# Kernel optimization log

Hardware: AMD Instinct MI355X
Metric: run time of the kernel (lower is better)

The kernel has to match this reference:

```python
import jax, jax.numpy as jnp
import numpy as np

N = 3072      # packed vision tokens (multiple of _BLOCK=128, so no padding needed)
D = 1280      # hidden_size
H = 16        # num_heads
K = 80        # head_dim = D // H
NSEG = 8      # number of packed images/segments


def setup_inputs() -> dict:
    key = jax.random.key(0)
    ks = jax.random.split(key, 8)
    hidden_ND = jax.random.normal(ks[0], (N, D), jnp.float32)
    inner = jnp.sort(jax.random.randint(ks[1], (NSEG - 1,), 1, N)).astype(jnp.int32)
    cu_seqlens = jnp.concatenate([
        jnp.zeros((1,), jnp.int32), inner, jnp.full((1,), N, jnp.int32)])
    theta = jax.random.uniform(ks[2], (N, K), jnp.float32, 0.0, 2.0 * np.pi)
    cos_NK = jnp.cos(theta)
    sin_NK = jnp.sin(theta)
    sd = 1.0 / np.sqrt(D)  # lecun_normal-ish scale
    qkv_w = jax.random.normal(ks[3], (D, 3 * D), jnp.float32) * sd
    qkv_b = jax.random.normal(ks[4], (3 * D,), jnp.float32) * 0.01
    proj_w = jax.random.normal(ks[5], (D, D), jnp.float32) * sd
    proj_b = jax.random.normal(ks[6], (D,), jnp.float32) * 0.01
    return {"hidden_ND": hidden_ND, "cu_seqlens": cu_seqlens,
            "cos_NK": cos_NK, "sin_NK": sin_NK,
            "qkv_w": qkv_w, "qkv_b": qkv_b,
            "proj_w": proj_w, "proj_b": proj_b}


def _rotate_half(x):
    x1, x2 = jnp.split(x, 2, axis=-1)
    return jnp.concatenate([-x2, x1], axis=-1)


def _apply_vision_rope(q_NHK, k_NHK, cos_NK, sin_NK):
    c = cos_NK[:, None, :]  # (N, 1, K) broadcast over heads
    s = sin_NK[:, None, :]
    q = q_NHK * c + _rotate_half(q_NHK) * s
    k = k_NHK * c + _rotate_half(k_NHK) * s
    return q, k


def reference(hidden_ND, cu_seqlens, cos_NK, sin_NK, qkv_w, qkv_b, proj_w, proj_b):
    n = hidden_ND.shape[0]
    scale = K ** (-0.5)
    qkv = (hidden_ND @ qkv_w + qkv_b).reshape(n, 3, H, K)
    q_NHK, k_NHK, v_NHK = qkv[:, 0], qkv[:, 1], qkv[:, 2]
    q_NHK, k_NHK = _apply_vision_rope(q_NHK, k_NHK, cos_NK, sin_NK)

    # segment-boundary mask: token i attends to [k_start[i], k_end[i])
    idx = jnp.arange(n)
    seg = jnp.searchsorted(cu_seqlens[1:], idx, side='right')
    nseg = cu_seqlens.shape[0]
    k_start = cu_seqlens[jnp.minimum(seg, nseg - 2)]
    k_end = cu_seqlens[jnp.minimum(seg + 1, nseg - 1)]
    mask = (idx[None, :] >= k_start[:, None]) & (idx[None, :] < k_end[:, None])  # (Nq, Nk)

    scores = jnp.einsum('nhk,mhk->hnm', q_NHK, k_NHK) * scale  # (H, N, N)
    scores = jnp.where(mask[None], scores, jnp.float32(-1e30))
    probs = jax.nn.softmax(scores, axis=-1)
    attn = jnp.einsum('hnm,mhk->nhk', probs, v_NHK)  # (N, H, K)
    out_ND = attn.reshape(n, H * K) @ proj_w + proj_b
    return out_ND
```

## Files before the change

kernel.cpp:

```cpp
#include <hip/hip_runtime.h>

#define NTOK 3072
#define DM   1280
#define NH   16
#define HD   80
#define HDS  104
#define KVB  128
#define NSEG 8
#define QKVC 3840

typedef __attribute__((ext_vector_type(4))) float  f32x4;
typedef __attribute__((ext_vector_type(8))) __bf16 bf16x8;
typedef __attribute__((ext_vector_type(8))) unsigned short ushort8;
typedef __attribute__((ext_vector_type(4))) unsigned short ushort4v;

static __device__ __forceinline__ unsigned short f2bf(float f){
  union{float f; unsigned int u;} v; v.f=f;
  unsigned int r = v.u + 0x7fffu + ((v.u>>16)&1u);
  return (unsigned short)(r>>16);
}
static __device__ __forceinline__ float bf2f(unsigned short u){
  union{unsigned int i; float f;} v; v.i = ((unsigned int)u)<<16; return v.f;
}
static __device__ __forceinline__ void gload_lds16(const void* g, void* l){
  __builtin_amdgcn_global_load_lds((const __attribute__((address_space(1))) void*)g,
                                   (__attribute__((address_space(3))) void*)l, 16, 0, 0);
}

__global__ void cast_f32_bf16(const float* __restrict__ src, unsigned short* __restrict__ dst, int n){
  int i = (blockIdx.x*256 + threadIdx.x)*4;
  if (i >= n) return;
  f32x4 v = *reinterpret_cast<const f32x4*>(&src[i]);
  ushort4v o;
  o[0]=f2bf(v[0]); o[1]=f2bf(v[1]); o[2]=f2bf(v[2]); o[3]=f2bf(v[3]);
  *reinterpret_cast<ushort4v*>(&dst[i]) = o;
}

__global__ void transpose_cast(const float* __restrict__ src, unsigned short* __restrict__ dst, int R, int C){
  __shared__ unsigned short tile[32][33];
  int c0 = blockIdx.x*32, r0 = blockIdx.y*32;
  int tx = threadIdx.x, ty = threadIdx.y;
  #pragma unroll
  for (int i=0;i<4;i++){
    int r = r0 + ty + i*8;
    tile[ty+i*8][tx] = f2bf(src[(size_t)r*C + c0 + tx]);
  }
  __syncthreads();
  #pragma unroll
  for (int i=0;i<4;i++){
    int c = c0 + ty + i*8;
    dst[(size_t)c*R + r0 + tx] = tile[tx][ty+i*8];
  }
}

__global__ void transpose_v(const unsigned short* __restrict__ qkv, unsigned short* __restrict__ Vt){
  __shared__ unsigned short tile[32][33];
  int n0 = blockIdx.x*32, d0 = blockIdx.y*32, h = blockIdx.z;
  int tx = threadIdx.x, ty = threadIdx.y;
  #pragma unroll
  for (int i=0;i<4;i++){
    int n = n0 + ty + i*8;
    int d = d0 + tx;
    tile[ty+i*8][tx] = (d < HD) ? qkv[(size_t)n*QKVC + 2*DM + h*HD + d] : (unsigned short)0;
  }
  __syncthreads();
  #pragma unroll
  for (int i=0;i<4;i++){
    int d = d0 + ty + i*8;
    if (d < HD) Vt[((size_t)h*HD + d)*NTOK + n0 + tx] = tile[tx][ty+i*8];
  }
}

template<int OUT_BF16>
__global__ __launch_bounds__(256) void gemm_bt(
    const unsigned short* __restrict__ A,
    const unsigned short* __restrict__ Bt,
    const float* __restrict__ bias,
    unsigned short* __restrict__ Cb,
    float* __restrict__ Cf,
    int M, int Ncol, int Kd)
{
  __shared__ unsigned short As[128*32];
  __shared__ unsigned short Bs[128*32];
  const int tid  = threadIdx.x;
  const int lane = tid & 63, wave = tid >> 6;
  const int wr = wave >> 1, wc = wave & 1;
  const int bm = blockIdx.y, bn = blockIdx.x;
  const f32x4 vzero = {0.f,0.f,0.f,0.f};

  f32x4 acc[4][4];
  #pragma unroll
  for (int i=0;i<4;i++)
    #pragma unroll
    for (int j=0;j<4;j++) acc[i][j] = vzero;

  const int rsub = lane>>2;
  const int kc   = (lane&3)*8;
  const unsigned short* Ab = A  + (size_t)(bm*128 + wave*32 + rsub)*Kd + kc;
  const unsigned short* Bb = Bt + (size_t)(bn*128 + wave*32 + rsub)*Kd + kc;

  for (int k0=0; k0<Kd; k0+=32){
    __syncthreads();
    #pragma unroll
    for (int i=0;i<2;i++){
      gload_lds16(Ab + (size_t)i*16*Kd + k0, &As[(wave*2+i)*512]);
      gload_lds16(Bb + (size_t)i*16*Kd + k0, &Bs[(wave*2+i)*512]);
    }
    __syncthreads();
    bf16x8 a[4], b[4];
    #pragma unroll
    for (int mf=0; mf<4; mf++)
      a[mf] = *reinterpret_cast<const bf16x8*>(&As[(wr*64 + mf*16 + (lane&15))*32 + ((lane>>4)<<3)]);
    #pragma unroll
    for (int nf=0; nf<4; nf++)
      b[nf] = *reinterpret_cast<const bf16x8*>(&Bs[(wc*64 + nf*16 + (lane&15))*32 + ((lane>>4)<<3)]);
    #pragma unroll
    for (int mf=0; mf<4; mf++)
      #pragma unroll
      for (int nf=0; nf<4; nf++)
        acc[mf][nf] = __builtin_amdgcn_mfma_f32_16x16x32_bf16(a[mf], b[nf], acc[mf][nf], 0,0,0);
  }

  const int crow0 = bm*128 + wr*64;
  const int ccol0 = bn*128 + wc*64;
  #pragma unroll
  for (int nf=0; nf<4; nf++){
    int col = ccol0 + nf*16 + (lane&15);
    float bv = bias[col];
    #pragma unroll
    for (int mf=0; mf<4; mf++){
      #pragma unroll
      for (int r=0;r<4;r++){
        int row = crow0 + mf*16 + ((lane>>4)<<2) + r;
        float v = acc[mf][nf][r] + bv;
        if (OUT_BF16) Cb[(size_t)row*Ncol + col] = f2bf(v);
        else          Cf[(size_t)row*Ncol + col] = v;
      }
    }
  }
}

__global__ void rope_repack(const unsigned short* __restrict__ qkv,
                            const float* __restrict__ cosNK, const float* __restrict__ sinNK,
                            unsigned short* __restrict__ Qr, unsigned short* __restrict__ Kr)
{
  int idx = blockIdx.x*256 + threadIdx.x;
  if (idx >= NH*NTOK*HDS) return;
  int k  = idx % HDS;
  int nh = idx / HDS;
  int n  = nh % NTOK;
  int h  = nh / NTOK;
  size_t dsti = (size_t)(h*NTOK + n)*HDS + k;
  if (k >= HD){ Qr[dsti]=0; Kr[dsti]=0; return; }
  float c = cosNK[n*HD + k], s = sinNK[n*HD + k];
  int   kp  = (k < 40) ? (k+40) : (k-40);
  float sgn = (k < 40) ? -1.f : 1.f;
  size_t base = (size_t)n*QKVC + h*HD;
  float q   = bf2f(qkv[base + k]);
  float qp  = bf2f(qkv[base + kp]);
  float kk  = bf2f(qkv[base + DM + k]);
  float kkp = bf2f(qkv[base + DM + kp]);
  Qr[dsti] = f2bf(q*c  + sgn*qp*s);
  Kr[dsti] = f2bf(kk*c + sgn*kkp*s);
}

__global__ __launch_bounds__(256) void attn_kernel(
    const unsigned short* __restrict__ Qr,
    const unsigned short* __restrict__ Kr,
    const unsigned short* __restrict__ Vt,
    const int* __restrict__ cu,
    unsigned short* __restrict__ attn_out)
{
  __shared__ unsigned short Qs[64*HDS];
  __shared__ unsigned short Ks[KVB*HDS];
  __shared__ unsigned short Vs[HD*KVB];
  __shared__ unsigned short Ps[64*KVB];
  __shared__ int rs[64], re[64];

  const int h   = blockIdx.y;
  const int q0  = blockIdx.x*64;
  const int tid = threadIdx.x;
  const int lane = tid & 63, wave = tid >> 6;
  const int l16 = lane & 15, g16 = lane >> 4;
  const f32x4 vzero = {0.f,0.f,0.f,0.f};

  if (tid < 64){
    int row = q0 + tid, seg = 0;
    #pragma unroll
    for (int j=1;j<NSEG;j++) seg += (cu[j] <= row) ? 1 : 0;
    rs[tid] = cu[seg]; re[tid] = cu[seg+1];
  }
  {
    const char* src = (const char*)(Qr + (size_t)(h*NTOK + q0)*HDS);
    #pragma unroll
    for (int i=0;i<4;i++){
      int t = tid + i*256;
      if (t < 832) gload_lds16(src + (size_t)t*16, (char*)Qs + (size_t)t*16);
    }
  }
  __syncthreads();
  const int kmin = rs[0], kmax = re[63];

  f32x4 accO[5];
  #pragma unroll
  for (int i=0;i<5;i++) accO[i] = vzero;
  float m_r[4] = {-1e30f,-1e30f,-1e30f,-1e30f};
  float l_r[4] = {0.f,0.f,0.f,0.f};
  const float scale = 0.11180339887498948f;

  for (int kt = (kmin/KVB)*KVB; kt < kmax; kt += KVB){
    __syncthreads();
    {
      const char* src = (const char*)(Kr + (size_t)(h*NTOK + kt)*HDS);
      #pragma unroll
      for (int i=0;i<7;i++){
        int t = tid + i*256;
        if (t < 1664) gload_lds16(src + (size_t)t*16, (char*)Ks + (size_t)t*16);
      }
    }
    {
      #pragma unroll
      for (int i=0;i<5;i++){
        int t = tid + i*256;
        int row = t >> 4;
        int ch  = (t & 15) ^ (row & 7);
        const unsigned short* src = Vt + ((size_t)h*HD + row)*NTOK + kt + ch*8;
        gload_lds16(src, (char*)Vs + (size_t)t*16);
      }
    }
    __syncthreads();

    f32x4 accS[8];
    #pragma unroll
    for (int i=0;i<8;i++) accS[i] = vzero;
    #pragma unroll
    for (int ks=0; ks<3; ks++){
      bf16x8 aq = *reinterpret_cast<const bf16x8*>((const char*)Qs + (wave*16 + l16)*208 + ks*64 + g16*16);
      #pragma unroll
      for (int nf=0;nf<8;nf++){
        bf16x8 bk = *reinterpret_cast<const bf16x8*>((const char*)Ks + (nf*16 + l16)*208 + ks*64 + g16*16);
        accS[nf] = __builtin_amdgcn_mfma_f32_16x16x32_bf16(aq, bk, accS[nf], 0,0,0);
      }
    }
    #pragma unroll
    for (int r=0;r<4;r++){
      const int row_i = wave*16 + g16*4 + r;
      const int rst = rs[row_i], ren = re[row_i];
      float sv[8]; bool ok[8];
      float mx = -1e30f;
      #pragma unroll
      for (int nf=0;nf<8;nf++){
        int kcol = kt + nf*16 + l16;
        ok[nf] = (kcol >= rst) && (kcol < ren);
        sv[nf] = accS[nf][r]*scale;
        if (ok[nf]) mx = fmaxf(mx, sv[nf]);
      }
      #pragma unroll
      for (int d=1; d<16; d<<=1) mx = fmaxf(mx, __shfl_xor(mx, d, 64));
      float mnew  = fmaxf(m_r[r], mx);
      float alpha = __expf(m_r[r] - mnew);
      m_r[r] = mnew;
      float lsum = 0.f;
      #pragma unroll
      for (int nf=0;nf<8;nf++){
        float p = ok[nf] ? __expf(sv[nf] - mnew) : 0.f;
        int pb = (row_i*256 + nf*32 + l16*2) ^ ((row_i&7)<<4);
        *reinterpret_cast<unsigned short*>((char*)Ps + pb) = f2bf(p);
        lsum += p;
      }
      #pragma unroll
      for (int d=1; d<16; d<<=1) lsum += __shfl_xor(lsum, d, 64);
      l_r[r] = l_r[r]*alpha + lsum;
      #pragma unroll
      for (int cf=0; cf<5; cf++) accO[cf][r] *= alpha;
    }
    #pragma unroll
    for (int ks=0; ks<4; ks++){
      const int arow = wave*16 + l16;
      bf16x8 ap = *reinterpret_cast<const bf16x8*>((char*)Ps + ((arow*256 + ks*64 + g16*16) ^ ((arow&7)<<4)));
      #pragma unroll
      for (int cf=0; cf<5; cf++){
        const int vrow = cf*16 + l16;
        bf16x8 bv = *reinterpret_cast<const bf16x8*>((char*)Vs + ((vrow*256 + ks*64 + g16*16) ^ ((vrow&7)<<4)));
        accO[cf] = __builtin_amdgcn_mfma_f32_16x16x32_bf16(ap, bv, accO[cf], 0,0,0);
      }
    }
  }

  #pragma unroll
  for (int cf=0; cf<5; cf++){
    #pragma unroll
    for (int r=0;r<4;r++){
      int row = q0 + wave*16 + g16*4 + r;
      int col = h*HD + cf*16 + l16;
      attn_out[(size_t)row*DM + col] = f2bf(accO[cf][r] / l_r[r]);
    }
  }
}

extern "C" void kernel_launch(void* const* d_in, const int* in_sizes, int n_in,
                              void* d_out, int out_size, void* d_ws, size_t ws_size,
                              hipStream_t stream)
{
  const float* hidden = (const float*)d_in[0];
  const int*   cu     = (const int*)  d_in[1];
  const float* cosNK  = (const float*)d_in[2];
  const float* sinNK  = (const float*)d_in[3];
  const float* qkv_w  = (const float*)d_in[4];
  const float* qkv_b  = (const float*)d_in[5];
  const float* proj_w = (const float*)d_in[6];
  const float* proj_b = (const float*)d_in[7];
  float* out = (float*)d_out;

  char* w = (char*)d_ws;
  unsigned short* hid_bf  = (unsigned short*)w;  w += (size_t)NTOK*DM*2;
  unsigned short* qkvwT   = (unsigned short*)w;  w += (size_t)QKVC*DM*2;
  unsigned short* projwT  = (unsigned short*)w;  w += (size_t)DM*DM*2;
  unsigned short* qkv_bf  = (unsigned short*)w;  w += (size_t)NTOK*QKVC*2;
  unsigned short* Qr      = (unsigned short*)w;  w += (size_t)NH*NTOK*HDS*2;
  unsigned short* Kr      = (unsigned short*)w;  w += (size_t)NH*NTOK*HDS*2;
  unsigned short* Vt      = qkvwT;
  unsigned short* attn_bf = hid_bf;

  cast_f32_bf16<<<(NTOK*DM/4 + 255)/256, 256, 0, stream>>>(hidden, hid_bf, NTOK*DM);
  transpose_cast<<<dim3(QKVC/32, DM/32), dim3(32,8), 0, stream>>>(qkv_w, qkvwT, DM, QKVC);
  transpose_cast<<<dim3(DM/32,  DM/32), dim3(32,8), 0, stream>>>(proj_w, projwT, DM, DM);
  gemm_bt<1><<<dim3(QKVC/128, NTOK/128), 256, 0, stream>>>(hid_bf, qkvwT, qkv_b, qkv_bf, nullptr, NTOK, QKVC, DM);
  rope_repack<<<(NH*NTOK*HDS + 255)/256, 256, 0, stream>>>(qkv_bf, cosNK, sinNK, Qr, Kr);
  transpose_v<<<dim3(NTOK/32, 3, NH), dim3(32,8), 0, stream>>>(qkv_bf, Vt);
  attn_kernel<<<dim3(NTOK/64, NH), 256, 0, stream>>>(Qr, Kr, Vt, cu, attn_bf);
  gemm_bt<0><<<dim3(DM/128, NTOK/128), 256, 0, stream>>>(attn_bf, projwT, proj_b, nullptr, out, NTOK, DM, DM);
}
```

Measured before the change: 273.2 us.

## Double-buffer GEMM and attention K tiles; load V directly into registers

The GEMM now double-buffers its A/B LDS tiles, issuing the next k-slice's global-to-LDS loads before computing on the current one, so each iteration needs one barrier instead of two. The attention kernel halves the KV block to 64, double-buffers K in LDS with a prefetch of the next tile, and loads V fragments straight from global memory into registers instead of staging them through LDS. It also computes the key range from cu_seqlens directly. The aim is to hide global load latency behind MFMA work and cut barriers, at the cost of more LDS, more registers, more loop iterations, and uncoalesced per-lane V reads from global memory.

After: 268.2 us. No clear change (-1.8%).

```diff
diff --git a/kernel.cpp b/kernel.cpp
--- a/kernel.cpp
+++ b/kernel.cpp
@@ -5,7 +5,7 @@
 #define NH   16
 #define HD   80
 #define HDS  104
-#define KVB  128
+#define KVB  64
 #define NSEG 8
 #define QKVC 3840
 
@@ -80,8 +80,8 @@
     float* __restrict__ Cf,
     int M, int Ncol, int Kd)
 {
-  __shared__ unsigned short As[128*32];
-  __shared__ unsigned short Bs[128*32];
+  __shared__ unsigned short As[2][128*32];
+  __shared__ unsigned short Bs[2][128*32];
   const int tid  = threadIdx.x;
   const int lane = tid & 63, wave = tid >> 6;
   const int wr = wave >> 1, wc = wave & 1;
@@ -99,21 +99,43 @@
   const unsigned short* Ab = A  + (size_t)(bm*128 + wave*32 + rsub)*Kd + kc;
   const unsigned short* Bb = Bt + (size_t)(bn*128 + wave*32 + rsub)*Kd + kc;
 
-  for (int k0=0; k0<Kd; k0+=32){
+  #pragma unroll
+  for (int i=0;i<2;i++){
+    gload_lds16(Ab + (size_t)i*16*Kd, &As[0][(wave*2+i)*512]);
+    gload_lds16(Bb + (size_t)i*16*Kd, &Bs[0][(wave*2+i)*512]);
+  }
+  __syncthreads();
+
+  int cur = 0;
+  for (int k0=32; k0<Kd; k0+=32){
+    #pragma unroll
+    for (int i=0;i<2;i++){
+      gload_lds16(Ab + (size_t)i*16*Kd + k0, &As[cur^1][(wave*2+i)*512]);
+      gload_lds16(Bb + (size_t)i*16*Kd + k0, &Bs[cur^1][(wave*2+i)*512]);
+    }
+    bf16x8 a[4], b[4];
+    #pragma unroll
+    for (int mf=0; mf<4; mf++)
+      a[mf] = *reinterpret_cast<const bf16x8*>(&As[cur][(wr*64 + mf*16 + (lane&15))*32 + ((lane>>4)<<3)]);
+    #pragma unroll
+    for (int nf=0; nf<4; nf++)
+      b[nf] = *reinterpret_cast<const bf16x8*>(&Bs[cur][(wc*64 + nf*16 + (lane&15))*32 + ((lane>>4)<<3)]);
+    #pragma unroll
+    for (int mf=0; mf<4; mf++)
+      #pragma unroll
+      for (int nf=0; nf<4; nf++)
+        acc[mf][nf] = __builtin_amdgcn_mfma_f32_16x16x32_bf16(a[mf], b[nf], acc[mf][nf], 0,0,0);
     __syncthreads();
-    #pragma unroll
-    for (int i=0;i<2;i++){
-      gload_lds16(Ab + (size_t)i*16*Kd + k0, &As[(wave*2+i)*512]);
-      gload_lds16(Bb + (size_t)i*16*Kd + k0, &Bs[(wave*2+i)*512]);
-    }
-    __syncthreads();
+    cur ^= 1;
+  }
+  {
     bf16x8 a[4], b[4];
     #pragma unroll
     for (int mf=0; mf<4; mf++)
-      a[mf] = *reinterpret_cast<const bf16x8*>(&As[(wr*64 + mf*16 + (lane&15))*32 + ((lane>>4)<<3)]);
+      a[mf] = *reinterpret_cast<const bf16x8*>(&As[cur][(wr*64 + mf*16 + (lane&15))*32 + ((lane>>4)<<3)]);
     #pragma unroll
     for (int nf=0; nf<4; nf++)
-      b[nf] = *reinterpret_cast<const bf16x8*>(&Bs[(wc*64 + nf*16 + (lane&15))*32 + ((lane>>4)<<3)]);
+      b[nf] = *reinterpret_cast<const bf16x8*>(&Bs[cur][(wc*64 + nf*16 + (lane&15))*32 + ((lane>>4)<<3)]);
     #pragma unroll
     for (int mf=0; mf<4; mf++)
       #pragma unroll
@@ -172,8 +194,7 @@
     unsigned short* __restrict__ attn_out)
 {
   __shared__ unsigned short Qs[64*HDS];
-  __shared__ unsigned short Ks[KVB*HDS];
-  __shared__ unsigned short Vs[HD*KVB];
+  __shared__ unsigned short Ks[2][KVB*HDS];
   __shared__ unsigned short Ps[64*KVB];
   __shared__ int rs[64], re[64];
 
@@ -190,6 +211,16 @@
     for (int j=1;j<NSEG;j++) seg += (cu[j] <= row) ? 1 : 0;
     rs[tid] = cu[seg]; re[tid] = cu[seg+1];
   }
+  int seg0 = 0, seg1 = 0;
+  #pragma unroll
+  for (int j=1;j<NSEG;j++){
+    seg0 += (cu[j] <= q0) ? 1 : 0;
+    seg1 += (cu[j] <= q0+63) ? 1 : 0;
+  }
+  const int kmin = cu[seg0], kmax = cu[seg1+1];
+  const int kt0 = kmin & ~(KVB-1);
+  const int nt  = (kmax - kt0 + KVB-1)/KVB;
+
   {
     const char* src = (const char*)(Qr + (size_t)(h*NTOK + q0)*HDS);
     #pragma unroll
@@ -198,8 +229,15 @@
       if (t < 832) gload_lds16(src + (size_t)t*16, (char*)Qs + (size_t)t*16);
     }
   }
+  {
+    const char* src = (const char*)(Kr + (size_t)(h*NTOK + kt0)*HDS);
+    #pragma unroll
+    for (int i=0;i<4;i++){
+      int t = tid + i*256;
+      if (t < 832) gload_lds16(src + (size_t)t*16, (char*)Ks[0] + (size_t)t*16);
+    }
+  }
   __syncthreads();
-  const int kmin = rs[0], kmax = re[63];
 
   f32x4 accO[5];
   #pragma unroll
@@ -208,37 +246,35 @@
   float l_r[4] = {0.f,0.f,0.f,0.f};
   const float scale = 0.11180339887498948f;
 
-  for (int kt = (kmin/KVB)*KVB; kt < kmax; kt += KVB){
-    __syncthreads();
+  int cur = 0;
+  for (int it = 0; it < nt; ++it){
+    const int kt  = kt0 + it*KVB;
+    const int ktn = kt0 + ((it+1 < nt) ? (it+1) : (nt-1))*KVB;
     {
-      const char* src = (const char*)(Kr + (size_t)(h*NTOK + kt)*HDS);
-      #pragma unroll
-      for (int i=0;i<7;i++){
+      const char* src = (const char*)(Kr + (size_t)(h*NTOK + ktn)*HDS);
+      #pragma unroll
+      for (int i=0;i<4;i++){
         int t = tid + i*256;
-        if (t < 1664) gload_lds16(src + (size_t)t*16, (char*)Ks + (size_t)t*16);
-      }
-    }
-    {
-      #pragma unroll
-      for (int i=0;i<5;i++){
-        int t = tid + i*256;
-        int row = t >> 4;
-        int ch  = (t & 15) ^ (row & 7);
-        const unsigned short* src = Vt + ((size_t)h*HD + row)*NTOK + kt + ch*8;
-        gload_lds16(src, (char*)Vs + (size_t)t*16);
-      }
-    }
-    __syncthreads();
-
-    f32x4 accS[8];
-    #pragma unroll
-    for (int i=0;i<8;i++) accS[i] = vzero;
+        if (t < 832) gload_lds16(src + (size_t)t*16, (char*)Ks[cur^1] + (size_t)t*16);
+      }
+    }
+    ushort8 vreg[2][5];
+    #pragma unroll
+    for (int ks=0; ks<2; ks++)
+      #pragma unroll
+      for (int cf=0; cf<5; cf++)
+        vreg[ks][cf] = *reinterpret_cast<const ushort8*>(
+            &Vt[((size_t)h*HD + cf*16 + l16)*NTOK + kt + ks*32 + g16*8]);
+
+    f32x4 accS[4];
+    #pragma unroll
+    for (int i=0;i<4;i++) accS[i] = vzero;
     #pragma unroll
     for (int ks=0; ks<3; ks++){
       bf16x8 aq = *reinterpret_cast<const bf16x8*>((const char*)Qs + (wave*16 + l16)*208 + ks*64 + g16*16);
       #pragma unroll
-      for (int nf=0;nf<8;nf++){
-        bf16x8 bk = *reinterpret_cast<const bf16x8*>((const char*)Ks + (nf*16 + l16)*208 + ks*64 + g16*16);
+      for (int nf=0;nf<4;nf++){
+        bf16x8 bk = *reinterpret_cast<const bf16x8*>((const char*)Ks[cur] + (nf*16 + l16)*208 + ks*64 + g16*16);
         accS[nf] = __builtin_amdgcn_mfma_f32_16x16x32_bf16(aq, bk, accS[nf], 0,0,0);
       }
     }
@@ -246,10 +282,10 @@
     for (int r=0;r<4;r++){
       const int row_i = wave*16 + g16*4 + r;
       const int rst = rs[row_i], ren = re[row_i];
-      float sv[8]; bool ok[8];
+      float sv[4]; bool ok[4];
       float mx = -1e30f;
       #pragma unroll
-      for (int nf=0;nf<8;nf++){
+      for (int nf=0;nf<4;nf++){
         int kcol = kt + nf*16 + l16;
         ok[nf] = (kcol >= rst) && (kcol < ren);
         sv[nf] = accS[nf][r]*scale;
@@ -262,9 +298,9 @@
       m_r[r] = mnew;
       float lsum = 0.f;
       #pragma unroll
-      for (int nf=0;nf<8;nf++){
+      for (int nf=0;nf<4;nf++){
         float p = ok[nf] ? __expf(sv[nf] - mnew) : 0.f;
-        int pb = (row_i*256 + nf*32 + l16*2) ^ ((row_i&7)<<4);
+        int pb = (row_i*128 + nf*32 + l16*2) ^ ((row_i&7)<<4);
         *reinterpret_cast<unsigned short*>((char*)Ps + pb) = f2bf(p);
         lsum += p;
       }
@@ -275,16 +311,17 @@
       for (int cf=0; cf<5; cf++) accO[cf][r] *= alpha;
     }
     #pragma unroll
-    for (int ks=0; ks<4; ks++){
+    for (int ks=0; ks<2; ks++){
       const int arow = wave*16 + l16;
-      bf16x8 ap = *reinterpret_cast<const bf16x8*>((char*)Ps + ((arow*256 + ks*64 + g16*16) ^ ((arow&7)<<4)));
+      bf16x8 ap = *reinterpret_cast<const bf16x8*>((char*)Ps + ((arow*128 + ks*64 + g16*16) ^ ((arow&7)<<4)));
       #pragma unroll
       for (int cf=0; cf<5; cf++){
-        const int vrow = cf*16 + l16;
-        bf16x8 bv = *reinterpret_cast<const bf16x8*>((char*)Vs + ((vrow*256 + ks*64 + g16*16) ^ ((vrow&7)<<4)));
+        bf16x8 bv = __builtin_bit_cast(bf16x8, vreg[ks][cf]);
         accO[cf] = __builtin_amdgcn_mfma_f32_16x16x32_bf16(ap, bv, accO[cf], 0,0,0);
       }
     }
+    __syncthreads();
+    cur ^= 1;
   }
 
   #pragma unroll
```
